# Optimization experiments

Measured on AMD Instinct MI355X. Metric: run time of the kernel, lower is better.

Reference implementation:

```python
import jax, jax.numpy as jnp
import numpy as np

EPS = 0.07      # sinkhorn temperature
ITERS = 7       # sinkhorn iterations
TINY = 1e-8
NORM_EPS = 1e-12  # F.normalize default clamp


def setup_inputs() -> dict:
    key = jax.random.key(0)
    k1, k2 = jax.random.split(key)
    x = jax.random.normal(k1, (64, 2048, 24, 12), dtype=jnp.float32)
    anchors = jax.random.normal(k2, (2, 2048), dtype=jnp.float32) * 0.02
    return {"x": x, "anchors": anchors}


def reference(x, anchors):
    B, C, H, W = x.shape
    HW = H * W
    # tokens: (B, HW, C)
    X = x.reshape(B, C, HW).transpose(0, 2, 1)
    Xn = X / jnp.maximum(jnp.linalg.norm(X, axis=-1, keepdims=True), NORM_EPS)
    An = anchors / jnp.maximum(jnp.linalg.norm(anchors, axis=-1, keepdims=True), NORM_EPS)
    # cosine cost (B, HW, 2)
    Cmat = 1.0 - jnp.einsum('bhc,kc->bhk', Xn, An)
    Kmat = jnp.exp(-Cmat / max(EPS, TINY)) + TINY
    a = jnp.full((B, HW), 1.0 / HW, dtype=Kmat.dtype)
    b = jnp.full((B, 2), 0.5, dtype=Kmat.dtype)

    def step(carry, _):
        u, v = carry
        Kv = jnp.einsum('bhk,bk->bh', Kmat, v) + TINY
        u = a / Kv
        KTu = jnp.einsum('bhk,bh->bk', Kmat, u) + TINY
        v = b / KTu
        return (u, v), None

    u0 = jnp.ones((B, HW), dtype=Kmat.dtype)
    v0 = jnp.ones((B, 2), dtype=Kmat.dtype)
    (u, v), _ = jax.lax.scan(step, (u0, v0), None, length=ITERS)
    # transport plan and soft masks
    P = Kmat * u[:, :, None] * v[:, None, :]          # (B, HW, 2)
    m = (P * HW).transpose(0, 2, 1).reshape(B, 2, H, W)
    # masked pooling for both prototypes at once
    num = jnp.einsum('bchw,bkhw->bkc', x, m)           # (B, 2, C)
    den = m.sum(axis=(2, 3)) + 1e-6                    # (B, 2)
    c = num / den[:, :, None]
    c0_vec = c[:, 0][:, :, None, None]                 # (B, C, 1, 1)
    c1_vec = c[:, 1][:, :, None, None]
    return (c0_vec, c1_vec, m)
```

## Files before the change

kernel.cpp:

```cpp
#include <hip/hip_runtime.h>

#define B_    64
#define C_    2048
#define HW_   288
#define EPS_  0.07f
#define TINY_ 1e-8f

__global__ __launch_bounds__(256) void k1_partials(
    const float* __restrict__ x, const float* __restrict__ anchors,
    float* __restrict__ part, int nch, int cpc) {
  int bi = blockIdx.x;
  int b  = bi / nch;
  int ch = bi - b * nch;
  int t  = threadIdx.x;
  const float* xb  = x + ((size_t)b * C_ + (size_t)ch * cpc) * HW_;
  const float* a0p = anchors + ch * cpc;
  const float* a1p = anchors + C_ + ch * cpc;
  float ssq = 0.f, sd0 = 0.f, sd1 = 0.f;
  float ssqb = 0.f, sd0b = 0.f, sd1b = 0.f;
#pragma unroll 4
  for (int c = 0; c < cpc; ++c) {
    float a0 = a0p[c], a1 = a1p[c];
    float v = xb[(size_t)c * HW_ + t];
    ssq += v * v; sd0 += v * a0; sd1 += v * a1;
    if (t < HW_ - 256) {
      float w = xb[(size_t)c * HW_ + 256 + t];
      ssqb += w * w; sd0b += w * a0; sd1b += w * a1;
    }
  }
  int PS = gridDim.x * HW_;
  int base = bi * HW_ + t;
  part[base] = ssq; part[PS + base] = sd0; part[2 * PS + base] = sd1;
  if (t < HW_ - 256) {
    int base2 = bi * HW_ + 256 + t;
    part[base2] = ssqb; part[PS + base2] = sd0b; part[2 * PS + base2] = sd1b;
  }
}

__device__ __forceinline__ void block_reduce2(
    float& p0, float& p1, volatile float* red0, volatile float* red1,
    int t, int nw) {
  int lane = t & 63, wid = t >> 6;
#pragma unroll
  for (int off = 32; off >= 1; off >>= 1) {
    p0 += __shfl_down(p0, off);
    p1 += __shfl_down(p1, off);
  }
  __syncthreads();
  if (lane == 0) { red0[wid] = p0; red1[wid] = p1; }
  __syncthreads();
  float s0 = 0.f, s1 = 0.f;
  for (int w = 0; w < nw; ++w) { s0 += red0[w]; s1 += red1[w]; }
  p0 = s0; p1 = s1;
}

__global__ __launch_bounds__(320) void k2_sinkhorn(
    const float* __restrict__ part, const float* __restrict__ anchors,
    int nch, float* __restrict__ out_m, float* __restrict__ invden) {
  int b = blockIdx.x, t = threadIdx.x;
  __shared__ float red0[8], red1[8];
  const int nw = 5;

  float a0 = 0.f, a1 = 0.f;
  for (int c = t; c < C_; c += 320) {
    float q0 = anchors[c], q1 = anchors[C_ + c];
    a0 += q0 * q0; a1 += q1 * q1;
  }
  block_reduce2(a0, a1, red0, red1, t, nw);
  float ian0 = 1.0f / fmaxf(sqrtf(a0), 1e-12f);
  float ian1 = 1.0f / fmaxf(sqrtf(a1), 1e-12f);

  float K0 = 0.f, K1 = 0.f;
  if (t < HW_) {
    int PS = B_ * nch * HW_;
    float ssq = 0.f, d0 = 0.f, d1 = 0.f;
    for (int ch = 0; ch < nch; ++ch) {
      int base = (b * nch + ch) * HW_ + t;
      ssq += part[base]; d0 += part[PS + base]; d1 += part[2 * PS + base];
    }
    float ixn = 1.0f / fmaxf(sqrtf(ssq), 1e-12f);
    float cos0 = d0 * ixn * ian0;
    float cos1 = d1 * ixn * ian1;
    K0 = expf((cos0 - 1.0f) / EPS_) + TINY_;
    K1 = expf((cos1 - 1.0f) / EPS_) + TINY_;
  }

  float v0 = 1.f, v1 = 1.f, u = 0.f;
  for (int it = 0; it < 7; ++it) {
    if (t < HW_) u = (1.0f / (float)HW_) / (K0 * v0 + K1 * v1 + TINY_);
    float p0 = K0 * u, p1 = K1 * u;
    block_reduce2(p0, p1, red0, red1, t, nw);
    v0 = 0.5f / (p0 + TINY_);
    v1 = 0.5f / (p1 + TINY_);
  }

  float m0 = 0.f, m1 = 0.f;
  if (t < HW_) {
    m0 = K0 * u * v0 * (float)HW_;
    m1 = K1 * u * v1 * (float)HW_;
  }
  float q0 = m0, q1 = m1;
  block_reduce2(q0, q1, red0, red1, t, nw);
  if (t < HW_) {
    out_m[(b * 2 + 0) * HW_ + t] = m0;
    out_m[(b * 2 + 1) * HW_ + t] = m1;
  }
  if (t == 0) {
    invden[b * 2 + 0] = 1.0f / (q0 + 1e-6f);
    invden[b * 2 + 1] = 1.0f / (q1 + 1e-6f);
  }
}

__global__ __launch_bounds__(256) void k3_pool(
    const float* __restrict__ x, const float* __restrict__ m,
    const float* __restrict__ invden, float* __restrict__ out) {
  int bi = blockIdx.x;
  int b = bi >> 4, tile = bi & 15;
  int t = threadIdx.x, lane = t & 63, wid = t >> 6;
  __shared__ float sm0[HW_], sm1[HW_];
  __shared__ float sinv[2];
  for (int i = t; i < HW_; i += 256) {
    sm0[i] = m[(b * 2 + 0) * HW_ + i];
    sm1[i] = m[(b * 2 + 1) * HW_ + i];
  }
  if (t == 0) { sinv[0] = invden[b * 2]; sinv[1] = invden[b * 2 + 1]; }
  __syncthreads();

  float ma0[4], ma1[4], mb0[4], mb1[4];
#pragma unroll
  for (int j = 0; j < 4; ++j) {
    ma0[j] = sm0[4 * lane + j];
    ma1[j] = sm1[4 * lane + j];
  }
  bool tail = lane < 8;
#pragma unroll
  for (int j = 0; j < 4; ++j) {
    mb0[j] = tail ? sm0[256 + 4 * lane + j] : 0.f;
    mb1[j] = tail ? sm1[256 + 4 * lane + j] : 0.f;
  }
  float inv0 = sinv[0], inv1 = sinv[1];

  int c0 = tile * 128 + wid * 32;
  for (int r = 0; r < 32; ++r) {
    int c = c0 + r;
    const float4* xr = (const float4*)(x + ((size_t)b * C_ + c) * HW_);
    float4 xa = xr[lane];
    float acc0 = xa.x * ma0[0] + xa.y * ma0[1] + xa.z * ma0[2] + xa.w * ma0[3];
    float acc1 = xa.x * ma1[0] + xa.y * ma1[1] + xa.z * ma1[2] + xa.w * ma1[3];
    if (tail) {
      float4 xb = xr[64 + lane];
      acc0 += xb.x * mb0[0] + xb.y * mb0[1] + xb.z * mb0[2] + xb.w * mb0[3];
      acc1 += xb.x * mb1[0] + xb.y * mb1[1] + xb.z * mb1[2] + xb.w * mb1[3];
    }
#pragma unroll
    for (int off = 32; off >= 1; off >>= 1) {
      acc0 += __shfl_down(acc0, off);
      acc1 += __shfl_down(acc1, off);
    }
    if (lane == 0) {
      out[(size_t)b * C_ + c] = acc0 * inv0;
      out[(size_t)B_ * C_ + (size_t)b * C_ + c] = acc1 * inv1;
    }
  }
}

extern "C" void kernel_launch(void* const* d_in, const int* in_sizes, int n_in,
                              void* d_out, int out_size, void* d_ws, size_t ws_size,
                              hipStream_t stream) {
  const float* x       = (const float*)d_in[0];
  const float* anchors = (const float*)d_in[1];
  float* out = (float*)d_out;

  float* invden = (float*)d_ws;
  int nch = 16;
  while (nch > 1 && (size_t)(128 + 3 * B_ * nch * HW_) * sizeof(float) > ws_size)
    nch >>= 1;
  float* part = invden + 128;
  int cpc = C_ / nch;

  float* out_m = out + 2 * B_ * C_;

  k1_partials<<<B_ * nch, 256, 0, stream>>>(x, anchors, part, nch, cpc);
  k2_sinkhorn<<<B_, 320, 0, stream>>>(part, anchors, nch, out_m, invden);
  k3_pool<<<B_ * 16, 256, 0, stream>>>(x, out_m, invden, out);
}
```

Measured before the change: 298.1 us.

## Split channel reduction finer, add partial-reduce kernel, thread-per-channel pooling

```diff
diff --git a/kernel.cpp b/kernel.cpp
--- a/kernel.cpp
+++ b/kernel.cpp
@@ -6,35 +6,69 @@
 #define EPS_  0.07f
 #define TINY_ 1e-8f
 
+__device__ __forceinline__ void acc3(const float4 v, float a0, float a1,
+                                     float* ssq, float* sd0, float* sd1) {
+  ssq[0] += v.x * v.x; ssq[1] += v.y * v.y; ssq[2] += v.z * v.z; ssq[3] += v.w * v.w;
+  sd0[0] += v.x * a0;  sd0[1] += v.y * a0;  sd0[2] += v.z * a0;  sd0[3] += v.w * a0;
+  sd1[0] += v.x * a1;  sd1[1] += v.y * a1;  sd1[2] += v.z * a1;  sd1[3] += v.w * a1;
+}
+
 __global__ __launch_bounds__(256) void k1_partials(
     const float* __restrict__ x, const float* __restrict__ anchors,
     float* __restrict__ part, int nch, int cpc) {
   int bi = blockIdx.x;
-  int b  = bi / nch;
-  int ch = bi - b * nch;
-  int t  = threadIdx.x;
-  const float* xb  = x + ((size_t)b * C_ + (size_t)ch * cpc) * HW_;
-  const float* a0p = anchors + ch * cpc;
-  const float* a1p = anchors + C_ + ch * cpc;
-  float ssq = 0.f, sd0 = 0.f, sd1 = 0.f;
-  float ssqb = 0.f, sd0b = 0.f, sd1b = 0.f;
+  int nblk = nch >> 2;
+  int b  = bi / nblk;
+  int cg = bi - b * nblk;
+  int t = threadIdx.x, lane = t & 63, wid = t >> 6;
+  int ch = cg * 4 + wid;
+  int c0 = ch * cpc;
+  const float* xb = x + ((size_t)b * C_ + c0) * HW_;
+  bool tail = lane < 8;
+
+  float ssq[4] = {0,0,0,0}, sd0[4] = {0,0,0,0}, sd1[4] = {0,0,0,0};
+  float tsq[4] = {0,0,0,0}, td0[4] = {0,0,0,0}, td1[4] = {0,0,0,0};
+
 #pragma unroll 4
-  for (int c = 0; c < cpc; ++c) {
-    float a0 = a0p[c], a1 = a1p[c];
-    float v = xb[(size_t)c * HW_ + t];
-    ssq += v * v; sd0 += v * a0; sd1 += v * a1;
-    if (t < HW_ - 256) {
-      float w = xb[(size_t)c * HW_ + 256 + t];
-      ssqb += w * w; sd0b += w * a0; sd1b += w * a1;
+  for (int r = 0; r < cpc; ++r) {
+    const float4* xr = (const float4*)(xb + (size_t)r * HW_);
+    float a0 = anchors[c0 + r];
+    float a1 = anchors[C_ + c0 + r];
+    float4 xa = xr[lane];
+    acc3(xa, a0, a1, ssq, sd0, sd1);
+    if (tail) {
+      float4 xc = xr[64 + lane];
+      acc3(xc, a0, a1, tsq, td0, td1);
     }
   }
-  int PS = gridDim.x * HW_;
-  int base = bi * HW_ + t;
-  part[base] = ssq; part[PS + base] = sd0; part[2 * PS + base] = sd1;
-  if (t < HW_ - 256) {
-    int base2 = bi * HW_ + 256 + t;
-    part[base2] = ssqb; part[PS + base2] = sd0b; part[2 * PS + base2] = sd1b;
-  }
+
+  size_t PS = (size_t)B_ * nch * HW_;
+  float* base = part + (size_t)(b * nch + ch) * HW_;
+  float4* p0 = (float4*)base;
+  float4* p1 = (float4*)(base + PS);
+  float4* p2 = (float4*)(base + 2 * PS);
+  p0[lane] = make_float4(ssq[0], ssq[1], ssq[2], ssq[3]);
+  p1[lane] = make_float4(sd0[0], sd0[1], sd0[2], sd0[3]);
+  p2[lane] = make_float4(sd1[0], sd1[1], sd1[2], sd1[3]);
+  if (tail) {
+    p0[64 + lane] = make_float4(tsq[0], tsq[1], tsq[2], tsq[3]);
+    p1[64 + lane] = make_float4(td0[0], td0[1], td0[2], td0[3]);
+    p2[64 + lane] = make_float4(td1[0], td1[1], td1[2], td1[3]);
+  }
+}
+
+__global__ __launch_bounds__(256) void k1b_reduce(
+    const float* __restrict__ part, float* __restrict__ red, int nch) {
+  int idx = blockIdx.x * 256 + threadIdx.x;
+  int plane = idx / (B_ * HW_);
+  int rem = idx - plane * (B_ * HW_);
+  int b = rem / HW_;
+  int h = rem - b * HW_;
+  const float* p = part + (size_t)plane * B_ * nch * HW_ + (size_t)b * nch * HW_ + h;
+  float s = 0.f;
+#pragma unroll 8
+  for (int ch = 0; ch < nch; ++ch) s += p[(size_t)ch * HW_];
+  red[idx] = s;
 }
 
 __device__ __forceinline__ void block_reduce2(
@@ -55,8 +89,8 @@
 }
 
 __global__ __launch_bounds__(320) void k2_sinkhorn(
-    const float* __restrict__ part, const float* __restrict__ anchors,
-    int nch, float* __restrict__ out_m, float* __restrict__ invden) {
+    const float* __restrict__ red, const float* __restrict__ anchors,
+    float* __restrict__ out_m, float* __restrict__ invden) {
   int b = blockIdx.x, t = threadIdx.x;
   __shared__ float red0[8], red1[8];
   const int nw = 5;
@@ -72,12 +106,9 @@
 
   float K0 = 0.f, K1 = 0.f;
   if (t < HW_) {
-    int PS = B_ * nch * HW_;
-    float ssq = 0.f, d0 = 0.f, d1 = 0.f;
-    for (int ch = 0; ch < nch; ++ch) {
-      int base = (b * nch + ch) * HW_ + t;
-      ssq += part[base]; d0 += part[PS + base]; d1 += part[2 * PS + base];
-    }
+    float ssq = red[b * HW_ + t];
+    float d0  = red[B_ * HW_ + b * HW_ + t];
+    float d1  = red[2 * B_ * HW_ + b * HW_ + t];
     float ixn = 1.0f / fmaxf(sqrtf(ssq), 1e-12f);
     float cos0 = d0 * ixn * ian0;
     float cos1 = d1 * ixn * ian1;
@@ -115,52 +146,35 @@
     const float* __restrict__ x, const float* __restrict__ m,
     const float* __restrict__ invden, float* __restrict__ out) {
   int bi = blockIdx.x;
-  int b = bi >> 4, tile = bi & 15;
-  int t = threadIdx.x, lane = t & 63, wid = t >> 6;
-  __shared__ float sm0[HW_], sm1[HW_];
+  int b = bi >> 4, seg = bi & 15;
+  int t = threadIdx.x;
+  int lr = t >> 1, half = t & 1;
+  int c = seg * 128 + lr;
+
+  __shared__ float4 sm0[72], sm1[72];
   __shared__ float sinv[2];
-  for (int i = t; i < HW_; i += 256) {
-    sm0[i] = m[(b * 2 + 0) * HW_ + i];
-    sm1[i] = m[(b * 2 + 1) * HW_ + i];
-  }
-  if (t == 0) { sinv[0] = invden[b * 2]; sinv[1] = invden[b * 2 + 1]; }
+  if (t < 72)       sm0[t]      = ((const float4*)(m + (b * 2 + 0) * HW_))[t];
+  else if (t < 144) sm1[t - 72] = ((const float4*)(m + (b * 2 + 1) * HW_))[t - 72];
+  if (t == 0) { sinv[0] = invden[2 * b]; sinv[1] = invden[2 * b + 1]; }
   __syncthreads();
 
-  float ma0[4], ma1[4], mb0[4], mb1[4];
-#pragma unroll
-  for (int j = 0; j < 4; ++j) {
-    ma0[j] = sm0[4 * lane + j];
-    ma1[j] = sm1[4 * lane + j];
-  }
-  bool tail = lane < 8;
-#pragma unroll
-  for (int j = 0; j < 4; ++j) {
-    mb0[j] = tail ? sm0[256 + 4 * lane + j] : 0.f;
-    mb1[j] = tail ? sm1[256 + 4 * lane + j] : 0.f;
-  }
-  float inv0 = sinv[0], inv1 = sinv[1];
-
-  int c0 = tile * 128 + wid * 32;
-  for (int r = 0; r < 32; ++r) {
-    int c = c0 + r;
-    const float4* xr = (const float4*)(x + ((size_t)b * C_ + c) * HW_);
-    float4 xa = xr[lane];
-    float acc0 = xa.x * ma0[0] + xa.y * ma0[1] + xa.z * ma0[2] + xa.w * ma0[3];
-    float acc1 = xa.x * ma1[0] + xa.y * ma1[1] + xa.z * ma1[2] + xa.w * ma1[3];
-    if (tail) {
-      float4 xb = xr[64 + lane];
-      acc0 += xb.x * mb0[0] + xb.y * mb0[1] + xb.z * mb0[2] + xb.w * mb0[3];
-      acc1 += xb.x * mb1[0] + xb.y * mb1[1] + xb.z * mb1[2] + xb.w * mb1[3];
-    }
-#pragma unroll
-    for (int off = 32; off >= 1; off >>= 1) {
-      acc0 += __shfl_down(acc0, off);
-      acc1 += __shfl_down(acc1, off);
-    }
-    if (lane == 0) {
-      out[(size_t)b * C_ + c] = acc0 * inv0;
-      out[(size_t)B_ * C_ + (size_t)b * C_ + c] = acc1 * inv1;
-    }
+  const float4* xr = (const float4*)(x + ((size_t)b * C_ + c) * HW_) + half * 36;
+  const float4* w0p = sm0 + half * 36;
+  const float4* w1p = sm1 + half * 36;
+  float acc0 = 0.f, acc1 = 0.f;
+#pragma unroll 4
+  for (int i = 0; i < 36; ++i) {
+    float4 xa = xr[i];
+    float4 w0 = w0p[i];
+    float4 w1 = w1p[i];
+    acc0 += xa.x * w0.x + xa.y * w0.y + xa.z * w0.z + xa.w * w0.w;
+    acc1 += xa.x * w1.x + xa.y * w1.y + xa.z * w1.z + xa.w * w1.w;
+  }
+  acc0 += __shfl_down(acc0, 1);
+  acc1 += __shfl_down(acc1, 1);
+  if (half == 0) {
+    out[(size_t)b * C_ + c] = acc0 * sinv[0];
+    out[(size_t)B_ * C_ + (size_t)b * C_ + c] = acc1 * sinv[1];
   }
 }
 
@@ -172,15 +186,18 @@
   float* out = (float*)d_out;
 
   float* invden = (float*)d_ws;
-  int nch = 16;
-  while (nch > 1 && (size_t)(128 + 3 * B_ * nch * HW_) * sizeof(float) > ws_size)
+  float* red = invden + 128;
+  float* part = red + 3 * B_ * HW_;
+  int nch = 128;
+  while (nch > 4 &&
+         (size_t)(128 + 3 * B_ * HW_ + 3 * B_ * nch * HW_) * sizeof(float) > ws_size)
     nch >>= 1;
-  float* part = invden + 128;
   int cpc = C_ / nch;
 
   float* out_m = out + 2 * B_ * C_;
 
-  k1_partials<<<B_ * nch, 256, 0, stream>>>(x, anchors, part, nch, cpc);
-  k2_sinkhorn<<<B_, 320, 0, stream>>>(part, anchors, nch, out_m, invden);
+  k1_partials<<<B_ * (nch / 4), 256, 0, stream>>>(x, anchors, part, nch, cpc);
+  k1b_reduce<<<(3 * B_ * HW_) / 256, 256, 0, stream>>>(part, red, nch);
+  k2_sinkhorn<<<B_, 320, 0, stream>>>(red, anchors, out_m, invden);
   k3_pool<<<B_ * 16, 256, 0, stream>>>(x, out_m, invden, out);
 }
```

Result: faster. 266.2 us (-10.7%).
